# Kernel tuning notes

Hardware: AMD Instinct MI355X
Metric: run time of the kernel (lower is better)

## Reference

```python
import jax, jax.numpy as jnp
import numpy as np

B, S, H, NH = 2, 2048, 1024, 16
HD = H // NH
EPS = 1e-6

def rotate_half(x):
    x1, x2 = jnp.split(x, 2, axis=-1)
    return jnp.concatenate([-x2, x1], axis=-1)

def setup_inputs() -> dict:
    key = jax.random.key(0)
    ks = jax.random.split(key, 4)
    x = jax.random.normal(ks[0], (B, S, H), dtype=jnp.float32)
    # rotary angles
    inv_freq = 1.0 / (10000.0 ** (np.arange(0, HD, 2, dtype=np.float32) / HD))
    t = np.arange(S, dtype=np.float32)
    freqs = np.einsum('s,d->sd', t, inv_freq)
    emb = np.concatenate([freqs, freqs], axis=-1)  # [S, HD]
    cos = jnp.broadcast_to(jnp.cos(emb)[None], (B, S, HD)).astype(jnp.float32)
    sin = jnp.broadcast_to(jnp.sin(emb)[None], (B, S, HD)).astype(jnp.float32)
    attn_mask = jnp.broadcast_to(jnp.tril(jnp.ones((S, S), jnp.float32))[None], (B, S, S))
    W_uvqk = jax.random.normal(ks[1], (4 * H, H), dtype=jnp.float32) * (1.0 / np.sqrt(H))
    b_uvqk = jnp.zeros((4 * H,), jnp.float32)
    gate_w = jnp.ones((H,), jnp.float32)
    W_out = jax.random.normal(ks[2], (H, H), dtype=jnp.float32) * (1.0 / np.sqrt(H))
    b_out = jnp.zeros((H,), jnp.float32)
    return {"x": x, "cos": cos, "sin": sin, "attn_mask": attn_mask,
            "W_uvqk": W_uvqk, "b_uvqk": b_uvqk, "gate_w": gate_w,
            "W_out": W_out, "b_out": b_out}

def reference(x, cos, sin, attn_mask, W_uvqk, b_uvqk, gate_w, W_out, b_out):
    b, s, h = x.shape
    residual = x
    uvqk = jnp.einsum('bsh,oh->bso', x, W_uvqk) + b_uvqk
    u, v, q, k = jnp.split(uvqk, 4, axis=-1)
    u = jax.nn.silu(u)
    q = q.reshape(b, s, NH, HD)
    k = k.reshape(b, s, NH, HD)
    v = v.reshape(b, s, NH, HD)
    c = cos[:, :, None, :]  # [B,S,1,HD] broadcasts over heads
    sn = sin[:, :, None, :]
    q = q * c + rotate_half(q) * sn
    k = k * c + rotate_half(k) * sn
    # [B,NH,S,S] raw scores -> silu (no softmax) -> mask -> AV
    scores = jnp.einsum('bqnd,bknd->bnqk', q, k) / np.sqrt(HD).astype(np.float32)
    attn = jax.nn.silu(scores) * attn_mask[:, None, :, :]
    attn_out = jnp.einsum('bnqk,bknd->bqnd', attn, v).reshape(b, s, h)
    # RMSNorm (fp32) gating
    ao32 = attn_out.astype(jnp.float32)
    var = jnp.mean(ao32 * ao32, axis=-1, keepdims=True)
    normed = (gate_w * (ao32 * jax.lax.rsqrt(var + EPS))).astype(x.dtype)
    gated = normed * u
    out = jnp.einsum('bsh,oh->bso', gated, W_out) + b_out
    return residual + out
```

## Files before the change

kernel.cpp:

```cpp
#include <hip/hip_runtime.h>

typedef __attribute__((ext_vector_type(4))) float f32x4;
typedef __attribute__((ext_vector_type(8))) short short8;

static __device__ __forceinline__ unsigned short f2bf(float f) {
    union { float f; unsigned int u; } v; v.f = f;
    unsigned int r = v.u + 0x7FFFu + ((v.u >> 16) & 1u);
    return (unsigned short)(r >> 16);
}

static __device__ __forceinline__ float bf2f(unsigned short h) {
    union { unsigned int u; float f; } v; v.u = ((unsigned int)h) << 16;
    return v.f;
}

static __device__ __forceinline__ unsigned int cvt_pk_bf16(float lo, float hi) {
    unsigned int r;
    asm("v_cvt_pk_bf16_f32 %0, %1, %2" : "=v"(r) : "v"(lo), "v"(hi));
    return r;
}

static __device__ __forceinline__ void gload16(const void* g, void* l) {
    __builtin_amdgcn_global_load_lds(
        (const __attribute__((address_space(1))) unsigned int*)g,
        (__attribute__((address_space(3))) unsigned int*)l, 16, 0, 0);
}

static __device__ __forceinline__ void block_sync_raw() {
    asm volatile("" ::: "memory");
    __builtin_amdgcn_s_barrier();
    asm volatile("" ::: "memory");
}

__global__ __launch_bounds__(256) void k_convert(
    const float* __restrict__ x, const float* __restrict__ wu, const float* __restrict__ wo,
    unsigned short* __restrict__ xb, unsigned short* __restrict__ wub, unsigned short* __restrict__ wob)
{
    int i = blockIdx.x * 256 + threadIdx.x;
    const float* src; unsigned short* dst; int off;
    if (i < 1048576)       { src = x;  dst = xb;  off = i; }
    else if (i < 2097152)  { src = wu; dst = wub; off = i - 1048576; }
    else                   { src = wo; dst = wob; off = i - 2097152; }
    float4 v = reinterpret_cast<const float4*>(src)[off];
    ushort4 o;
    o.x = f2bf(v.x); o.y = f2bf(v.y); o.z = f2bf(v.z); o.w = f2bf(v.w);
    reinterpret_cast<ushort4*>(dst)[off] = o;
}

template<int MODE>
__global__ __launch_bounds__(256) void k_gemm(
    const unsigned short* __restrict__ A, const unsigned short* __restrict__ Bmat,
    const float* __restrict__ bias,
    unsigned short* __restrict__ u_out, unsigned short* __restrict__ q_out,
    unsigned short* __restrict__ k_out, unsigned short* __restrict__ vt_out,
    const float* __restrict__ cosp, const float* __restrict__ sinp,
    const float* __restrict__ resid, float* __restrict__ out)
{
    const int K = 1024;
    constexpr int NT = 16;
    constexpr int BM = (MODE == 0) ? 128 : 64;
    constexpr int MT = BM / 32;
    constexpr int ACH = BM / 32;
    constexpr int ASZ = BM * 64;
    constexpr int BSZ = 128 * 64;
    __shared__ __align__(16) unsigned short S[2 * (ASZ + BSZ)];
    int tid = threadIdx.x;
    int lane = tid & 63, wid = tid >> 6;
    int lo = lane & 15, q4 = lane >> 4;
    int x7 = lo & 7;
    int wr = wid >> 1, wc = wid & 1;
    int bn = blockIdx.x, bm = blockIdx.y;
    const unsigned short* Abase = A + (size_t)bm * BM * K;
    const unsigned short* Bbase = Bmat + (size_t)bn * 128 * K;

    auto stage = [&](int bb, int kt) {
        unsigned short* As = S + bb * (ASZ + BSZ);
        unsigned short* Bs = As + ASZ;
#pragma unroll
        for (int j = 0; j < ACH; ++j) {
            int ch = tid + j * 256;
            int r = ch >> 3, p = ch & 7;
            gload16(Abase + (size_t)r * K + kt * 64 + (p ^ (r & 7)) * 8, As + ch * 8);
        }
#pragma unroll
        for (int j = 0; j < 4; ++j) {
            int ch = tid + j * 256;
            int r = ch >> 3, p = ch & 7;
            gload16(Bbase + (size_t)r * K + kt * 64 + (p ^ (r & 7)) * 8, Bs + ch * 8);
        }
    };

    f32x4 acc[MT][4] = {};
    stage(0, 0);
    int buf = 0;
    for (int kt = 0; kt < NT; ++kt) {
        if (kt + 1 < NT) {
            stage(buf ^ 1, kt + 1);
            if constexpr (MODE == 0) { asm volatile("s_waitcnt vmcnt(8)" ::: "memory"); }
            else                     { asm volatile("s_waitcnt vmcnt(6)" ::: "memory"); }
        } else {
            asm volatile("s_waitcnt vmcnt(0)" ::: "memory");
        }
        block_sync_raw();
        const unsigned short* As = S + buf * (ASZ + BSZ);
        const unsigned short* Bs = As + ASZ;
#pragma unroll
        for (int kc = 0; kc < 2; ++kc) {
            short8 af[MT], bfr[4];
#pragma unroll
            for (int t = 0; t < MT; ++t)
                af[t] = *(const short8*)&As[(wr * (BM / 2) + t * 16 + lo) * 64 + (((kc * 4 + q4) ^ x7) * 8)];
#pragma unroll
            for (int t = 0; t < 4; ++t)
                bfr[t] = *(const short8*)&Bs[(wc * 64 + t * 16 + lo) * 64 + (((kc * 4 + q4) ^ x7) * 8)];
#pragma unroll
            for (int mt = 0; mt < MT; ++mt)
#pragma unroll
                for (int nt = 0; nt < 4; ++nt)
                    acc[mt][nt] = __builtin_amdgcn_mfma_f32_16x16x32_bf16(af[mt], bfr[nt], acc[mt][nt], 0, 0, 0);
        }
        block_sync_raw();
        buf ^= 1;
    }

    int rowb = bm * BM + wr * (BM / 2);
    int colb = bn * 128 + wc * 64;
    if (MODE == 0) {
        int region = colb >> 10;
        if (region == 1) {
            unsigned short* T = S;
#pragma unroll
            for (int mt = 0; mt < MT; ++mt)
#pragma unroll
                for (int nt = 0; nt < 4; ++nt) {
                    float bcol = bias[colb + nt * 16 + lo];
                    uint2 w;
                    w.x = cvt_pk_bf16(acc[mt][nt][0] + bcol, acc[mt][nt][1] + bcol);
                    w.y = cvt_pk_bf16(acc[mt][nt][2] + bcol, acc[mt][nt][3] + bcol);
                    int c_local = wc * 64 + nt * 16 + lo;
                    int schunk = wr * 8 + mt * 2 + (q4 >> 1);
                    *(uint2*)((char*)T + c_local * 256 + ((schunk ^ (c_local & 15)) * 16) + (q4 & 1) * 8) = w;
                }
            __syncthreads();
            int c_row = tid >> 1;
            int bchunk = (tid & 1) * 8;
            int c_global = (bn - 8) * 128 + c_row;
            int head = c_global >> 6, d = c_global & 63;
            int batch = (bm * 128) >> 11;
            unsigned short* vrow = vt_out + ((size_t)(batch * 16 + head) * 64 + d) * 2048;
#pragma unroll
            for (int i = 0; i < 8; ++i) {
                int chunk = bchunk + i;
                uint4 v = *(const uint4*)((const char*)T + c_row * 256 + ((chunk ^ (c_row & 15)) * 16));
                int s = (bm * 128 + chunk * 8) & 2047;
                *(uint4*)&vrow[s] = v;
            }
        } else {
#pragma unroll
            for (int mt = 0; mt < MT; ++mt) {
#pragma unroll
                for (int r = 0; r < 4; ++r) {
                    int rg = rowb + mt * 16 + q4 * 4 + r;
                    int b = rg >> 11, s = rg & 2047;
                    float vals[4];
#pragma unroll
                    for (int nt = 0; nt < 4; ++nt)
                        vals[nt] = acc[mt][nt][r] + bias[colb + nt * 16 + lo];
                    if (region == 0) {
#pragma unroll
                        for (int nt = 0; nt < 4; ++nt) {
                            float vv = vals[nt];
                            u_out[(size_t)rg * 1024 + colb + nt * 16 + lo] = f2bf(vv / (1.f + __expf(-vv)));
                        }
                    } else {
                        const float* cb = cosp + (size_t)(b * 2048 + s) * 64;
                        const float* sb = sinp + (size_t)(b * 2048 + s) * 64;
                        float o[4];
#pragma unroll
                        for (int nt = 0; nt < 4; ++nt) {
                            int hd = nt * 16 + lo;
                            float partner = (nt < 2) ? -vals[nt + 2] : vals[nt - 2];
                            o[nt] = vals[nt] * cb[hd] + partner * sb[hd];
                        }
                        int c0 = colb - ((region == 2) ? 2048 : 3072);
                        unsigned short* dst = (region == 2) ? q_out : k_out;
#pragma unroll
                        for (int nt = 0; nt < 4; ++nt) {
                            int c = c0 + nt * 16 + lo;
                            int head = c >> 6, d = c & 63;
                            dst[((size_t)(b * 16 + head) * 2048 + s) * 64 + d] = f2bf(o[nt]);
                        }
                    }
                }
            }
        }
    } else {
#pragma unroll
        for (int mt = 0; mt < MT; ++mt)
#pragma unroll
            for (int r = 0; r < 4; ++r) {
                int rg = rowb + mt * 16 + q4 * 4 + r;
#pragma unroll
                for (int nt = 0; nt < 4; ++nt) {
                    int c = colb + nt * 16 + lo;
                    out[(size_t)rg * 1024 + c] = acc[mt][nt][r] + bias[c] + resid[(size_t)rg * 1024 + c];
                }
            }
    }
}

__global__ __launch_bounds__(256) void k_attn(
    const unsigned short* __restrict__ Q, const unsigned short* __restrict__ Kg,
    const unsigned short* __restrict__ Vt_g, float* __restrict__ AO0, float* __restrict__ AO1)
{
    __shared__ __align__(16) unsigned short Ksb[2][64 * 64];
    __shared__ __align__(16) unsigned short Vsb[2][64 * 64];
    __shared__ __align__(16) unsigned short Ps[4 * 2048];
    int tid = threadIdx.x;
    int lane = tid & 63, wid = tid >> 6;
    int lo = lane & 15, q4 = lane >> 4;
    int bid = blockIdx.x;
    int bh = bid & 31;
    int s  = bid >> 5;
    int b = bh >> 4, head = bh & 15;

    const unsigned short* Qb = Q    + (size_t)bh * 2048 * 64;
    const unsigned short* Kb = Kg   + (size_t)bh * 2048 * 64;
    const unsigned short* Vb = Vt_g + (size_t)bh * 64 * 2048;
    unsigned short* Pw = Ps + wid * 2048;

    int i0 = wid * 128 + lane;
    int i1 = wid * 128 + 64 + lane;
    int c_0 = i0 & 7, r_0 = i0 >> 3;
    int c_1 = i1 & 7, r_1 = i1 >> 3;
    int cs0 = c_0 ^ (r_0 & 7), cs1 = c_1 ^ (r_1 & 7);
    size_t kOff0 = (size_t)r_0 * 64 + cs0 * 8,  kOff1 = (size_t)r_1 * 64 + cs1 * 8;
    size_t vOff0 = (size_t)r_0 * 2048 + cs0 * 8, vOff1 = (size_t)r_1 * 2048 + cs1 * 8;

    int x7 = lo & 7, qr_rel = q4 >> 1;
    char* pw0 = (char*)Pw + (lo)      * 128 + (q4 & 1) * 8;
    char* pw1 = (char*)Pw + (lo + 16) * 128 + (q4 & 1) * 8;
    int swz[8];
#pragma unroll
    for (int cc = 0; cc < 8; ++cc) swz[cc] = (cc ^ x7) * 16;
    const short8* prd[2][2];
#pragma unroll
    for (int kc = 0; kc < 2; ++kc) {
        prd[0][kc] = (const short8*)&Pw[(lo) * 64      + (((kc * 4 + q4) ^ x7) * 8)];
        prd[1][kc] = (const short8*)&Pw[(16 + lo) * 64 + (((kc * 4 + q4) ^ x7) * 8)];
    }

    auto stage = [&](int bb, int kt) {
        gload16(Kb + (size_t)kt * 4096 + kOff0, &Ksb[bb][i0 * 8]);
        gload16(Kb + (size_t)kt * 4096 + kOff1, &Ksb[bb][i1 * 8]);
        gload16(Vb + (size_t)kt * 64 + vOff0, &Vsb[bb][i0 * 8]);
        gload16(Vb + (size_t)kt * 64 + vOff1, &Vsb[bb][i1 * 8]);
    };

    int J = s;
    int q0w = J * 128 + wid * 32;
    short8 qf[2][2];
#pragma unroll
    for (int qt = 0; qt < 2; ++qt)
#pragma unroll
        for (int kc = 0; kc < 2; ++kc)
            qf[qt][kc] = *(const short8*)(Qb + (size_t)(q0w + qt * 16 + lo) * 64 + kc * 32 + q4 * 8);

    f32x4 oacc[2][4] = {};
    stage(0, 0);
    __syncthreads();
    int buf = 0;

    for (int t = 0; t < 17; ++t) {
        int kt = (t <= s) ? t : (t + 15 - 2 * s);
        if (t < 16) {
            int tn = t + 1;
            int ktn = (tn <= s) ? tn : (tn + 15 - 2 * s);
            stage(buf ^ 1, ktn);
        }
        if (64 * kt <= q0w + 31) {
            f32x4 sacc[4][2] = {};
#pragma unroll
            for (int kc = 0; kc < 2; ++kc)
#pragma unroll
                for (int kt4 = 0; kt4 < 4; ++kt4) {
                    short8 kf = *(const short8*)&Ksb[buf][(kt4 * 16 + lo) * 64 + (((kc * 4 + q4) ^ x7) * 8)];
#pragma unroll
                    for (int qt = 0; qt < 2; ++qt)
                        sacc[kt4][qt] = __builtin_amdgcn_mfma_f32_16x16x32_bf16(kf, qf[qt][kc], sacc[kt4][qt], 0, 0, 0);
                }
            bool needMask = (64 * kt + 63 > q0w);
#pragma unroll
            for (int kt4 = 0; kt4 < 4; ++kt4)
#pragma unroll
                for (int qt = 0; qt < 2; ++qt) {
                    int qc = qt * 16 + lo;
                    float p[4];
#pragma unroll
                    for (int rr = 0; rr < 4; ++rr) {
                        float S = sacc[kt4][qt][rr];
                        float e = __builtin_amdgcn_exp2f(S * -0.180336880f);
                        float pv = S * 0.125f * __builtin_amdgcn_rcpf(1.f + e);
                        if (needMask) {
                            int ky = kt * 64 + kt4 * 16 + q4 * 4 + rr;
                            if (ky > q0w + qc) pv = 0.f;
                        }
                        p[rr] = pv;
                    }
                    uint2 w;
                    w.x = cvt_pk_bf16(p[0], p[1]);
                    w.y = cvt_pk_bf16(p[2], p[3]);
                    *(uint2*)(((qt == 0) ? pw0 : pw1) + swz[kt4 * 2 + qr_rel]) = w;
                }
#pragma unroll
            for (int kc = 0; kc < 2; ++kc) {
                short8 pf0 = *prd[0][kc];
                short8 pf1 = *prd[1][kc];
#pragma unroll
                for (int nt = 0; nt < 4; ++nt) {
                    short8 vf = *(const short8*)&Vsb[buf][(nt * 16 + lo) * 64 + (((kc * 4 + q4) ^ x7) * 8)];
                    oacc[0][nt] = __builtin_amdgcn_mfma_f32_16x16x32_bf16(pf0, vf, oacc[0][nt], 0, 0, 0);
                    oacc[1][nt] = __builtin_amdgcn_mfma_f32_16x16x32_bf16(pf1, vf, oacc[1][nt], 0, 0, 0);
                }
            }
        }
        if (t == s) {
            float* aoLane = AO0 + ((size_t)(b * 2048 + q0w + q4 * 4)) * 1024 + head * 64 + lo;
#pragma unroll
            for (int qt = 0; qt < 2; ++qt)
#pragma unroll
                for (int nt = 0; nt < 4; ++nt)
#pragma unroll
                    for (int rr = 0; rr < 4; ++rr) {
                        aoLane[(qt * 16 + rr) * 1024 + nt * 16] = oacc[qt][nt][rr];
                        oacc[qt][nt][rr] = 0.f;
                    }
            J = 15 - s;
            q0w = J * 128 + wid * 32;
#pragma unroll
            for (int qt = 0; qt < 2; ++qt)
#pragma unroll
                for (int kc = 0; kc < 2; ++kc)
                    qf[qt][kc] = *(const short8*)(Qb + (size_t)(q0w + qt * 16 + lo) * 64 + kc * 32 + q4 * 8);
        }
        __syncthreads();
        buf ^= 1;
    }
    float* aoLane = AO1 + ((size_t)(b * 2048 + q0w + q4 * 4)) * 1024 + head * 64 + lo;
#pragma unroll
    for (int qt = 0; qt < 2; ++qt)
#pragma unroll
        for (int nt = 0; nt < 4; ++nt)
#pragma unroll
            for (int rr = 0; rr < 4; ++rr)
                aoLane[(qt * 16 + rr) * 1024 + nt * 16] = oacc[qt][nt][rr];
}

__global__ __launch_bounds__(256) void k_rmsgate(
    const float* __restrict__ AO0, const float* __restrict__ AO1, const unsigned short* __restrict__ U,
    const float* __restrict__ gw, unsigned short* __restrict__ G)
{
    __shared__ float red[4];
    int row = blockIdx.x, t = threadIdx.x;
    float4 a0 = *(const float4*)&AO0[(size_t)row * 1024 + t * 4];
    float4 a1 = *(const float4*)&AO1[(size_t)row * 1024 + t * 4];
    float4 a;
    a.x = a0.x + a1.x; a.y = a0.y + a1.y; a.z = a0.z + a1.z; a.w = a0.w + a1.w;
    float ss = a.x * a.x + a.y * a.y + a.z * a.z + a.w * a.w;
#pragma unroll
    for (int off = 32; off; off >>= 1) ss += __shfl_down(ss, off);
    int wid = t >> 6, lane = t & 63;
    if (lane == 0) red[wid] = ss;
    __syncthreads();
    float tot = red[0] + red[1] + red[2] + red[3];
    float rs = rsqrtf(tot * (1.f / 1024.f) + 1e-6f);
    float4 g = *(const float4*)&gw[t * 4];
    ushort4 uv = *(const ushort4*)&U[(size_t)row * 1024 + t * 4];
    ushort4 o;
    o.x = f2bf(g.x * a.x * rs * bf2f(uv.x));
    o.y = f2bf(g.y * a.y * rs * bf2f(uv.y));
    o.z = f2bf(g.z * a.z * rs * bf2f(uv.z));
    o.w = f2bf(g.w * a.w * rs * bf2f(uv.w));
    *(ushort4*)&G[(size_t)row * 1024 + t * 4] = o;
}

extern "C" void kernel_launch(void* const* d_in, const int* in_sizes, int n_in,
                              void* d_out, int out_size, void* d_ws, size_t ws_size,
                              hipStream_t stream) {
    const float* x      = (const float*)d_in[0];
    const float* cosp   = (const float*)d_in[1];
    const float* sinp   = (const float*)d_in[2];
    const float* b_uvqk = (const float*)d_in[5];
    const float* gate_w = (const float*)d_in[6];
    const float* b_out  = (const float*)d_in[8];
    float* out = (float*)d_out;

    char* ws = (char*)d_ws;
    unsigned short* xb  = (unsigned short*)(ws);
    unsigned short* wub = (unsigned short*)(ws + 8388608);
    unsigned short* wob = (unsigned short*)(ws + 16777216);
    unsigned short* ub  = (unsigned short*)(ws + 18874368);
    unsigned short* qb  = (unsigned short*)(ws + 35651584);
    unsigned short* kb  = (unsigned short*)(ws + 44040192);
    unsigned short* vtb = (unsigned short*)(ws + 52428800);
    float*          aob = (float*)(ws + 60817408);
    unsigned short* gb  = (unsigned short*)(ws + 77594624);
    float*          ao1 = (float*)(ws);

    k_convert<<<9216, 256, 0, stream>>>((const float*)d_in[0], (const float*)d_in[4],
                                        (const float*)d_in[7], xb, wub, wob);
    k_gemm<0><<<dim3(32, 32), 256, 0, stream>>>(xb, wub, b_uvqk, ub, qb, kb, vtb,
                                                cosp, sinp, nullptr, nullptr);
    k_attn<<<512, 256, 0, stream>>>(qb, kb, vtb, aob, ao1);
    k_rmsgate<<<4096, 256, 0, stream>>>(aob, ao1, ub, gate_w, gb);
    k_gemm<1><<<dim3(8, 64), 256, 0, stream>>>(gb, wob, b_out, nullptr, nullptr, nullptr, nullptr,
                                               nullptr, nullptr, x, out);
}
```

Measured before the change: 127.8 us.

## Use 256x256 tiles with 512-thread blocks for the QKV projection GEMM

Splits the templated GEMM into two kernels and enlarges the first projection GEMM tile to 256x256 with 8 waves per block, giving exactly one block per CU. The larger tile doubles operand reuse from shared memory and reduces global traffic; the V transpose epilogue is adapted to the wider tile. It trades occupancy (one block per CU, large LDS and register footprint) for reuse, which may reduce latency hiding.

```diff
diff --git a/kernel.cpp b/kernel.cpp
--- a/kernel.cpp
+++ b/kernel.cpp
@@ -47,21 +47,156 @@
     reinterpret_cast<ushort4*>(dst)[off] = o;
 }
 
-template<int MODE>
-__global__ __launch_bounds__(256) void k_gemm(
+__global__ __launch_bounds__(512, 1) void k_gemm0(
     const unsigned short* __restrict__ A, const unsigned short* __restrict__ Bmat,
     const float* __restrict__ bias,
     unsigned short* __restrict__ u_out, unsigned short* __restrict__ q_out,
     unsigned short* __restrict__ k_out, unsigned short* __restrict__ vt_out,
-    const float* __restrict__ cosp, const float* __restrict__ sinp,
-    const float* __restrict__ resid, float* __restrict__ out)
+    const float* __restrict__ cosp, const float* __restrict__ sinp)
 {
     const int K = 1024;
     constexpr int NT = 16;
-    constexpr int BM = (MODE == 0) ? 128 : 64;
-    constexpr int MT = BM / 32;
-    constexpr int ACH = BM / 32;
-    constexpr int ASZ = BM * 64;
+    constexpr int ASZ = 256 * 64;
+    constexpr int BSZ = 256 * 64;
+    __shared__ __align__(16) unsigned short S[2 * (ASZ + BSZ)];
+    int tid = threadIdx.x;
+    int lane = tid & 63, wid = tid >> 6;
+    int lo = lane & 15, q4 = lane >> 4;
+    int x7 = lo & 7;
+    int wr = wid >> 2, wc = wid & 3;
+    int bn = blockIdx.x, bm = blockIdx.y;
+    const unsigned short* Abase = A + (size_t)bm * 256 * K;
+    const unsigned short* Bbase = Bmat + (size_t)bn * 256 * K;
+
+    auto stage = [&](int bb, int kt) {
+        unsigned short* As = S + bb * (ASZ + BSZ);
+        unsigned short* Bs = As + ASZ;
+#pragma unroll
+        for (int j = 0; j < 4; ++j) {
+            int ch = tid + j * 512;
+            int r = ch >> 3, p = ch & 7;
+            gload16(Abase + (size_t)r * K + kt * 64 + (p ^ (r & 7)) * 8, As + ch * 8);
+        }
+#pragma unroll
+        for (int j = 0; j < 4; ++j) {
+            int ch = tid + j * 512;
+            int r = ch >> 3, p = ch & 7;
+            gload16(Bbase + (size_t)r * K + kt * 64 + (p ^ (r & 7)) * 8, Bs + ch * 8);
+        }
+    };
+
+    f32x4 acc[8][4] = {};
+    stage(0, 0);
+    int buf = 0;
+    for (int kt = 0; kt < NT; ++kt) {
+        if (kt + 1 < NT) {
+            stage(buf ^ 1, kt + 1);
+            asm volatile("s_waitcnt vmcnt(8)" ::: "memory");
+        } else {
+            asm volatile("s_waitcnt vmcnt(0)" ::: "memory");
+        }
+        block_sync_raw();
+        const unsigned short* As = S + buf * (ASZ + BSZ);
+        const unsigned short* Bs = As + ASZ;
+#pragma unroll
+        for (int kc = 0; kc < 2; ++kc) {
+            int cRd = (kc * 4 + q4) ^ x7;
+            short8 af[8], bfr[4];
+#pragma unroll
+            for (int t = 0; t < 8; ++t)
+                af[t] = *(const short8*)&As[(wr * 128 + t * 16 + lo) * 64 + cRd * 8];
+#pragma unroll
+            for (int t = 0; t < 4; ++t)
+                bfr[t] = *(const short8*)&Bs[(wc * 64 + t * 16 + lo) * 64 + cRd * 8];
+#pragma unroll
+            for (int mt = 0; mt < 8; ++mt)
+#pragma unroll
+                for (int nt = 0; nt < 4; ++nt)
+                    acc[mt][nt] = __builtin_amdgcn_mfma_f32_16x16x32_bf16(af[mt], bfr[nt], acc[mt][nt], 0, 0, 0);
+        }
+        block_sync_raw();
+        buf ^= 1;
+    }
+
+    int rowb = bm * 256 + wr * 128;
+    int colb = bn * 256 + wc * 64;
+    int region = bn >> 2;
+    if (region == 1) {
+        unsigned short* T = S;
+#pragma unroll
+        for (int mt = 0; mt < 8; ++mt)
+#pragma unroll
+            for (int nt = 0; nt < 4; ++nt) {
+                float bcol = bias[colb + nt * 16 + lo];
+                uint2 w;
+                w.x = cvt_pk_bf16(acc[mt][nt][0] + bcol, acc[mt][nt][1] + bcol);
+                w.y = cvt_pk_bf16(acc[mt][nt][2] + bcol, acc[mt][nt][3] + bcol);
+                int c_local = wc * 64 + nt * 16 + lo;
+                int schunk = wr * 16 + mt * 2 + (q4 >> 1);
+                *(uint2*)((char*)T + c_local * 512 + ((schunk ^ (c_local & 31)) * 16) + (q4 & 1) * 8) = w;
+            }
+        __syncthreads();
+        int c_row = tid >> 1;
+        int bchunk = (tid & 1) * 16;
+        int c_global = (bn - 4) * 256 + c_row;
+        int head = c_global >> 6, d = c_global & 63;
+        int batch = bm >> 3;
+        int s_base = (bm * 256) & 2047;
+        unsigned short* vrow = vt_out + ((size_t)(batch * 16 + head) * 64 + d) * 2048;
+#pragma unroll
+        for (int i = 0; i < 16; ++i) {
+            int chunk = bchunk + i;
+            uint4 v = *(const uint4*)((const char*)T + c_row * 512 + ((chunk ^ (c_row & 31)) * 16));
+            *(uint4*)&vrow[s_base + chunk * 8] = v;
+        }
+    } else {
+#pragma unroll
+        for (int mt = 0; mt < 8; ++mt) {
+#pragma unroll
+            for (int r = 0; r < 4; ++r) {
+                int rg = rowb + mt * 16 + q4 * 4 + r;
+                int b = rg >> 11, s = rg & 2047;
+                float vals[4];
+#pragma unroll
+                for (int nt = 0; nt < 4; ++nt)
+                    vals[nt] = acc[mt][nt][r] + bias[colb + nt * 16 + lo];
+                if (region == 0) {
+#pragma unroll
+                    for (int nt = 0; nt < 4; ++nt) {
+                        float vv = vals[nt];
+                        u_out[(size_t)rg * 1024 + colb + nt * 16 + lo] = f2bf(vv / (1.f + __expf(-vv)));
+                    }
+                } else {
+                    const float* cb = cosp + (size_t)(b * 2048 + s) * 64;
+                    const float* sb = sinp + (size_t)(b * 2048 + s) * 64;
+                    float o[4];
+#pragma unroll
+                    for (int nt = 0; nt < 4; ++nt) {
+                        int hd = nt * 16 + lo;
+                        float partner = (nt < 2) ? -vals[nt + 2] : vals[nt - 2];
+                        o[nt] = vals[nt] * cb[hd] + partner * sb[hd];
+                    }
+                    int c0 = colb - ((region == 2) ? 2048 : 3072);
+                    unsigned short* dst = (region == 2) ? q_out : k_out;
+#pragma unroll
+                    for (int nt = 0; nt < 4; ++nt) {
+                        int c = c0 + nt * 16 + lo;
+                        int head = c >> 6, d = c & 63;
+                        dst[((size_t)(b * 16 + head) * 2048 + s) * 64 + d] = f2bf(o[nt]);
+                    }
+                }
+            }
+        }
+    }
+}
+
+__global__ __launch_bounds__(256) void k_gemm1(
+    const unsigned short* __restrict__ A, const unsigned short* __restrict__ Bmat,
+    const float* __restrict__ bias, const float* __restrict__ resid, float* __restrict__ out)
+{
+    const int K = 1024;
+    constexpr int NT = 16;
+    constexpr int ASZ = 64 * 64;
     constexpr int BSZ = 128 * 64;
     __shared__ __align__(16) unsigned short S[2 * (ASZ + BSZ)];
     int tid = threadIdx.x;
@@ -70,14 +205,14 @@
     int x7 = lo & 7;
     int wr = wid >> 1, wc = wid & 1;
     int bn = blockIdx.x, bm = blockIdx.y;
-    const unsigned short* Abase = A + (size_t)bm * BM * K;
+    const unsigned short* Abase = A + (size_t)bm * 64 * K;
     const unsigned short* Bbase = Bmat + (size_t)bn * 128 * K;
 
     auto stage = [&](int bb, int kt) {
         unsigned short* As = S + bb * (ASZ + BSZ);
         unsigned short* Bs = As + ASZ;
 #pragma unroll
-        for (int j = 0; j < ACH; ++j) {
+        for (int j = 0; j < 2; ++j) {
             int ch = tid + j * 256;
             int r = ch >> 3, p = ch & 7;
             gload16(Abase + (size_t)r * K + kt * 64 + (p ^ (r & 7)) * 8, As + ch * 8);
@@ -90,14 +225,13 @@
         }
     };
 
-    f32x4 acc[MT][4] = {};
+    f32x4 acc[2][4] = {};
     stage(0, 0);
     int buf = 0;
     for (int kt = 0; kt < NT; ++kt) {
         if (kt + 1 < NT) {
             stage(buf ^ 1, kt + 1);
-            if constexpr (MODE == 0) { asm volatile("s_waitcnt vmcnt(8)" ::: "memory"); }
-            else                     { asm volatile("s_waitcnt vmcnt(6)" ::: "memory"); }
+            asm volatile("s_waitcnt vmcnt(6)" ::: "memory");
         } else {
             asm volatile("s_waitcnt vmcnt(0)" ::: "memory");
         }
@@ -106,15 +240,16 @@
         const unsigned short* Bs = As + ASZ;
 #pragma unroll
         for (int kc = 0; kc < 2; ++kc) {
-            short8 af[MT], bfr[4];
-#pragma unroll
-            for (int t = 0; t < MT; ++t)
-                af[t] = *(const short8*)&As[(wr * (BM / 2) + t * 16 + lo) * 64 + (((kc * 4 + q4) ^ x7) * 8)];
+            int cRd = (kc * 4 + q4) ^ x7;
+            short8 af[2], bfr[4];
+#pragma unroll
+            for (int t = 0; t < 2; ++t)
+                af[t] = *(const short8*)&As[(wr * 32 + t * 16 + lo) * 64 + cRd * 8];
 #pragma unroll
             for (int t = 0; t < 4; ++t)
-                bfr[t] = *(const short8*)&Bs[(wc * 64 + t * 16 + lo) * 64 + (((kc * 4 + q4) ^ x7) * 8)];
-#pragma unroll
-            for (int mt = 0; mt < MT; ++mt)
+                bfr[t] = *(const short8*)&Bs[(wc * 64 + t * 16 + lo) * 64 + cRd * 8];
+#pragma unroll
+            for (int mt = 0; mt < 2; ++mt)
 #pragma unroll
                 for (int nt = 0; nt < 4; ++nt)
                     acc[mt][nt] = __builtin_amdgcn_mfma_f32_16x16x32_bf16(af[mt], bfr[nt], acc[mt][nt], 0, 0, 0);
@@ -123,90 +258,19 @@
         buf ^= 1;
     }
 
-    int rowb = bm * BM + wr * (BM / 2);
+    int rowb = bm * 64 + wr * 32;
     int colb = bn * 128 + wc * 64;
-    if (MODE == 0) {
-        int region = colb >> 10;
-        if (region == 1) {
-            unsigned short* T = S;
-#pragma unroll
-            for (int mt = 0; mt < MT; ++mt)
-#pragma unroll
-                for (int nt = 0; nt < 4; ++nt) {
-                    float bcol = bias[colb + nt * 16 + lo];
-                    uint2 w;
-                    w.x = cvt_pk_bf16(acc[mt][nt][0] + bcol, acc[mt][nt][1] + bcol);
-                    w.y = cvt_pk_bf16(acc[mt][nt][2] + bcol, acc[mt][nt][3] + bcol);
-                    int c_local = wc * 64 + nt * 16 + lo;
-                    int schunk = wr * 8 + mt * 2 + (q4 >> 1);
-                    *(uint2*)((char*)T + c_local * 256 + ((schunk ^ (c_local & 15)) * 16) + (q4 & 1) * 8) = w;
-                }
-            __syncthreads();
-            int c_row = tid >> 1;
-            int bchunk = (tid & 1) * 8;
-            int c_global = (bn - 8) * 128 + c_row;
-            int head = c_global >> 6, d = c_global & 63;
-            int batch = (bm * 128) >> 11;
-            unsigned short* vrow = vt_out + ((size_t)(batch * 16 + head) * 64 + d) * 2048;
-#pragma unroll
-            for (int i = 0; i < 8; ++i) {
-                int chunk = bchunk + i;
-                uint4 v = *(const uint4*)((const char*)T + c_row * 256 + ((chunk ^ (c_row & 15)) * 16));
-                int s = (bm * 128 + chunk * 8) & 2047;
-                *(uint4*)&vrow[s] = v;
+#pragma unroll
+    for (int mt = 0; mt < 2; ++mt)
+#pragma unroll
+        for (int r = 0; r < 4; ++r) {
+            int rg = rowb + mt * 16 + q4 * 4 + r;
+#pragma unroll
+            for (int nt = 0; nt < 4; ++nt) {
+                int c = colb + nt * 16 + lo;
+                out[(size_t)rg * 1024 + c] = acc[mt][nt][r] + bias[c] + resid[(size_t)rg * 1024 + c];
             }
-        } else {
-#pragma unroll
-            for (int mt = 0; mt < MT; ++mt) {
-#pragma unroll
-                for (int r = 0; r < 4; ++r) {
-                    int rg = rowb + mt * 16 + q4 * 4 + r;
-                    int b = rg >> 11, s = rg & 2047;
-                    float vals[4];
-#pragma unroll
-                    for (int nt = 0; nt < 4; ++nt)
-                        vals[nt] = acc[mt][nt][r] + bias[colb + nt * 16 + lo];
-                    if (region == 0) {
-#pragma unroll
-                        for (int nt = 0; nt < 4; ++nt) {
-                            float vv = vals[nt];
-                            u_out[(size_t)rg * 1024 + colb + nt * 16 + lo] = f2bf(vv / (1.f + __expf(-vv)));
-                        }
-                    } else {
-                        const float* cb = cosp + (size_t)(b * 2048 + s) * 64;
-                        const float* sb = sinp + (size_t)(b * 2048 + s) * 64;
-                        float o[4];
-#pragma unroll
-                        for (int nt = 0; nt < 4; ++nt) {
-                            int hd = nt * 16 + lo;
-                            float partner = (nt < 2) ? -vals[nt + 2] : vals[nt - 2];
-                            o[nt] = vals[nt] * cb[hd] + partner * sb[hd];
-                        }
-                        int c0 = colb - ((region == 2) ? 2048 : 3072);
-                        unsigned short* dst = (region == 2) ? q_out : k_out;
-#pragma unroll
-                        for (int nt = 0; nt < 4; ++nt) {
-                            int c = c0 + nt * 16 + lo;
-                            int head = c >> 6, d = c & 63;
-                            dst[((size_t)(b * 16 + head) * 2048 + s) * 64 + d] = f2bf(o[nt]);
-                        }
-                    }
-                }
-            }
-        }
-    } else {
-#pragma unroll
-        for (int mt = 0; mt < MT; ++mt)
-#pragma unroll
-            for (int r = 0; r < 4; ++r) {
-                int rg = rowb + mt * 16 + q4 * 4 + r;
-#pragma unroll
-                for (int nt = 0; nt < 4; ++nt) {
-                    int c = colb + nt * 16 + lo;
-                    out[(size_t)rg * 1024 + c] = acc[mt][nt][r] + bias[c] + resid[(size_t)rg * 1024 + c];
-                }
-            }
-    }
+        }
 }
 
 __global__ __launch_bounds__(256) void k_attn(
@@ -409,10 +473,8 @@
 
     k_convert<<<9216, 256, 0, stream>>>((const float*)d_in[0], (const float*)d_in[4],
                                         (const float*)d_in[7], xb, wub, wob);
-    k_gemm<0><<<dim3(32, 32), 256, 0, stream>>>(xb, wub, b_uvqk, ub, qb, kb, vtb,
-                                                cosp, sinp, nullptr, nullptr);
+    k_gemm0<<<dim3(16, 16), 512, 0, stream>>>(xb, wub, b_uvqk, ub, qb, kb, vtb, cosp, sinp);
     k_attn<<<512, 256, 0, stream>>>(qb, kb, vtb, aob, ao1);
     k_rmsgate<<<4096, 256, 0, stream>>>(aob, ao1, ub, gate_w, gb);
-    k_gemm<1><<<dim3(8, 64), 256, 0, stream>>>(gb, wob, b_out, nullptr, nullptr, nullptr, nullptr,
-                                               nullptr, nullptr, x, out);
-}
+    k_gemm1<<<dim3(8, 64), 256, 0, stream>>>(gb, wob, b_out, x, out);
+}
```

New measurement: 122.1 us. 4.5% less time.
